# Kernel tuning notes

Hardware: AMD Instinct MI355X
Metric: run time of the kernel (lower is better)

Reference implementation:

```python
import jax, jax.numpy as jnp
import numpy as np

HEADS = 8
DIM_HEAD = 64

def setup_inputs() -> dict:
    key = jax.random.key(0)
    k1, k2, k3 = jax.random.split(key, 3)
    B, L, D = 8, 4096, 512
    hidden = HEADS * DIM_HEAD  # 512
    x = jax.random.normal(k1, (B, L, D), dtype=jnp.float32)
    # Conv1d(kernel_size=1) weights, squeezed to 2D matrices
    Wqkv = jax.random.normal(k2, (3 * hidden, D), dtype=jnp.float32) * (1.0 / np.sqrt(D))
    Wout = jax.random.normal(k3, (D, hidden), dtype=jnp.float32) * (1.0 / np.sqrt(hidden))
    bout = jnp.zeros((D,), dtype=jnp.float32)
    return {"x": x, "Wqkv": Wqkv, "Wout": Wout, "bout": bout}

def reference(x, Wqkv, Wout, bout):
    B, L, D = x.shape
    H, C = HEADS, DIM_HEAD
    # pointwise conv == linear over channel dim: (b, 3*H*C, l)
    qkv = jnp.einsum('bld,od->bol', x, Wqkv)
    qkv = qkv.reshape(B, 3, H, C, L)  # channel split order: (qkv, heads, c)
    q, k, v = qkv[:, 0], qkv[:, 1], qkv[:, 2]  # each (b, h, c, l)
    k = jax.nn.softmax(k, axis=-1)   # softmax over sequence
    q = jax.nn.softmax(q, axis=-2)   # softmax over feature dim (q_norm=True)
    context = jnp.einsum('bhdn,bhen->bhde', k, v)   # (b,h,c,c)
    out = jnp.einsum('bhde,bhdn->bhen', context, q)  # (b,h,c,l)
    out = out.reshape(B, H * C, L)
    y = jnp.einsum('bcl,dc->bld', out, Wout) + bout  # to_out + permute back
    return y
```

## Files before the change

kernel.cpp:

```cpp
#include <hip/hip_runtime.h>

#define L 4096
#define D 512
#define NCH 16

typedef __bf16 bf16x8 __attribute__((ext_vector_type(8)));
typedef float  f32x4  __attribute__((ext_vector_type(4)));

__device__ __forceinline__ void load_lds16(const void* g, void* l) {
    __builtin_amdgcn_global_load_lds(
        (const __attribute__((address_space(1))) void*)g,
        (__attribute__((address_space(3))) void*)l, 16, 0, 0);
}

__device__ __forceinline__ void barrier_mem() {
    asm volatile("" ::: "memory");
    __builtin_amdgcn_s_barrier();
    asm volatile("" ::: "memory");
}

#define NX8  (8 * 4096 * 512 / 8)
#define NW18 (1536 * 512 / 8)
#define NW28 (512 * 512 / 8)
__global__ __launch_bounds__(256) void convert_all(const float* __restrict__ x,
                                                   const float* __restrict__ Wq,
                                                   const float* __restrict__ Wo,
                                                   __bf16* __restrict__ dst) {
    int i = blockIdx.x * 256 + threadIdx.x;
    if (i >= NX8 + NW18 + NW28) return;
    const float* s;
    if (i < NX8)             s = x  + (size_t)i * 8;
    else if (i < NX8 + NW18) s = Wq + (size_t)(i - NX8) * 8;
    else                     s = Wo + (size_t)(i - NX8 - NW18) * 8;
    float4 a = ((const float4*)s)[0], b = ((const float4*)s)[1];
    bf16x8 o = {(__bf16)a.x, (__bf16)a.y, (__bf16)a.z, (__bf16)a.w,
                (__bf16)b.x, (__bf16)b.y, (__bf16)b.z, (__bf16)b.w};
    *(bf16x8*)(dst + (size_t)i * 8) = o;
}

template <int M, int N, int K, typename CT>
__global__ __launch_bounds__(512, 2) void gemm_bf16_256(
    const __bf16* __restrict__ A, size_t aStride,
    const __bf16* __restrict__ B, size_t bStride,
    CT* __restrict__ C, size_t cStride,
    const float* __restrict__ bias) {
    __shared__ __align__(16) __bf16 sA[2][256 * 64];
    __shared__ __align__(16) __bf16 sB[2][256 * 64];
    const int b  = blockIdx.z;
    const int m0 = blockIdx.y * 256;
    const int n0 = blockIdx.x * 256;
    const int t    = threadIdx.x;
    const int wave = t >> 6, lane = t & 63;
    const int wm = (wave >> 2) * 128;
    const int wn = (wave & 3) * 64;
    const int fr = lane & 15, g = lane >> 4;
    const __bf16* Ab = A + (size_t)b * aStride;
    const __bf16* Bb = B + (size_t)b * bStride;
    CT* Cb = C + (size_t)b * cStride;

    f32x4 acc[8][4];
#pragma unroll
    for (int i = 0; i < 8; i++)
#pragma unroll
        for (int j = 0; j < 4; j++) acc[i][j] = (f32x4)(0.0f);

    constexpr int NT = K / 64;

    auto stage2 = [&](int it, int kt, int pb) {
        const int idx = it * 512 + t;
        const int row = idx >> 3, cc = idx & 7;
        const int scc = cc ^ (row & 7);
        const size_t off = (size_t)row * K + (size_t)kt * 64 + scc * 8;
        load_lds16(Ab + (size_t)m0 * K + off, &sA[pb][idx * 8]);
        load_lds16(Bb + (size_t)n0 * K + off, &sB[pb][idx * 8]);
    };
    auto rdA4 = [&](bf16x8* dst, int pb, int ib, int kh) {
#pragma unroll
        for (int i = 0; i < 4; ++i) {
            const int row = wm + (ib + i) * 16 + fr;
            dst[i] = *(const bf16x8*)&sA[pb][row * 64 + (((kh << 2) + g) ^ (fr & 7)) * 8];
        }
    };
    auto rdB4 = [&](bf16x8* dst, int pb, int kh) {
#pragma unroll
        for (int j = 0; j < 4; ++j) {
            const int row = wn + j * 16 + fr;
            dst[j] = *(const bf16x8*)&sB[pb][row * 64 + (((kh << 2) + g) ^ (fr & 7)) * 8];
        }
    };
    auto mm16 = [&](const bf16x8* af, const bf16x8* bfr, int ib) {
        __builtin_amdgcn_s_setprio(1);
#pragma unroll
        for (int i = 0; i < 4; ++i)
#pragma unroll
            for (int j = 0; j < 4; ++j)
                acc[ib + i][j] = __builtin_amdgcn_mfma_f32_16x16x32_bf16(
                    af[i], bfr[j], acc[ib + i][j], 0, 0, 0);
        __builtin_amdgcn_s_setprio(0);
    };

#pragma unroll
    for (int it = 0; it < 4; ++it) stage2(it, 0, 0);

    for (int kt = 0; kt < NT; ++kt) {
        const int p = kt & 1;
        const bool pf = (kt + 1 < NT);
        bf16x8 bl[4], bh[4], al[4], ah[4], al2[4], ah2[4];

        if (pf) {
            stage2(0, kt + 1, p ^ 1);
            asm volatile("s_waitcnt vmcnt(2)" ::: "memory");
        } else {
            asm volatile("s_waitcnt vmcnt(0)" ::: "memory");
        }
        barrier_mem();
        rdB4(bl, p, 0);
        rdA4(al, p, 0, 0);
        rdA4(ah, p, 4, 0);
        asm volatile("s_waitcnt lgkmcnt(4)" ::: "memory");
        __builtin_amdgcn_sched_barrier(0);
        mm16(al, bl, 0);
        if (pf) stage2(1, kt + 1, p ^ 1);
        barrier_mem();

        rdB4(bh, p, 1);
        rdA4(al2, p, 0, 1);
        asm volatile("s_waitcnt lgkmcnt(8)" ::: "memory");
        __builtin_amdgcn_sched_barrier(0);
        mm16(ah, bl, 4);
        if (pf) stage2(2, kt + 1, p ^ 1);
        barrier_mem();

        rdA4(ah2, p, 4, 1);
        asm volatile("s_waitcnt lgkmcnt(4)" ::: "memory");
        __builtin_amdgcn_sched_barrier(0);
        mm16(al2, bh, 0);
        if (pf) stage2(3, kt + 1, p ^ 1);
        barrier_mem();

        asm volatile("s_waitcnt lgkmcnt(0)" ::: "memory");
        __builtin_amdgcn_sched_barrier(0);
        mm16(ah2, bh, 4);
        barrier_mem();
    }

    const int rb = g * 4;
#pragma unroll
    for (int j = 0; j < 4; ++j) {
        const int n = n0 + wn + j * 16 + fr;
        const float bv = bias ? bias[n] : 0.0f;
#pragma unroll
        for (int i = 0; i < 8; ++i) {
#pragma unroll
            for (int r = 0; r < 4; ++r) {
                const int m = m0 + wm + i * 16 + rb + r;
                Cb[(size_t)m * N + n] = (CT)(acc[i][j][r] + bv);
            }
        }
    }
}

__global__ __launch_bounds__(256) void kstats(const __bf16* __restrict__ qkv,
                                              float2* __restrict__ stats) {
    const int r = blockIdx.x;
    const int b = r >> 9, hc = r & 511;
    const __bf16* row = qkv + (size_t)b * 1536 * L + (size_t)(512 + hc) * L;
    __shared__ float sred[4];
    const int t = threadIdx.x;
    const bf16x8* p = (const bf16x8*)row;
    bf16x8 c0 = p[t * 2], c1 = p[t * 2 + 1];
    float v[16];
    float m = -1e30f;
#pragma unroll
    for (int j = 0; j < 8; j++) {
        v[j] = (float)c0[j];
        v[8 + j] = (float)c1[j];
    }
#pragma unroll
    for (int j = 0; j < 16; j++) m = fmaxf(m, v[j]);
#pragma unroll
    for (int off = 32; off > 0; off >>= 1) m = fmaxf(m, __shfl_down(m, off, 64));
    if ((t & 63) == 0) sred[t >> 6] = m;
    __syncthreads();
    const float m4 = fmaxf(fmaxf(sred[0], sred[1]), fmaxf(sred[2], sred[3]));
    float s = 0.f;
#pragma unroll
    for (int j = 0; j < 16; j++) s += __expf(v[j] - m4);
#pragma unroll
    for (int off = 32; off > 0; off >>= 1) s += __shfl_down(s, off, 64);
    __syncthreads();
    if ((t & 63) == 0) sred[t >> 6] = s;
    __syncthreads();
    if (t == 0) {
        const float stot = sred[0] + sred[1] + sred[2] + sred[3];
        stats[r] = make_float2(m4, 1.0f / stot);
    }
}

#define SKS 264
__global__ __launch_bounds__(256) void context_mfma(const __bf16* __restrict__ qkv,
                                                    const float2* __restrict__ stats,
                                                    float* __restrict__ ctxp) {
    __shared__ __align__(16) __bf16 smem[2 * 64 * SKS];
    __shared__ float smax[64];
    __bf16* sk = smem;
    __bf16* sv = smem + 64 * SKS;
    const int chunk = blockIdx.x;
    const int bh = blockIdx.y;
    const int b = bh >> 3, h = bh & 7;
    const __bf16* kbase = qkv + (size_t)b * 1536 * L + (size_t)(512 + h * 64) * L;
    const __bf16* vbase = qkv + (size_t)b * 1536 * L + (size_t)(1024 + h * 64) * L;
    const int t = threadIdx.x;
    if (t < 64) smax[t] = stats[bh * 64 + t].x;
    __syncthreads();

    {
        const int d = t >> 2, noff = (t & 3) * 64;
        const int n0 = chunk * 256;
        const __bf16* kp = kbase + (size_t)d * L + n0 + noff;
        const __bf16* vp = vbase + (size_t)d * L + n0 + noff;
        const float md = smax[d];
#pragma unroll
        for (int c = 0; c < 8; c++) {
            bf16x8 kk = *(const bf16x8*)(kp + c * 8);
            bf16x8 vv = *(const bf16x8*)(vp + c * 8);
            bf16x8 ek;
#pragma unroll
            for (int j = 0; j < 8; j++) ek[j] = (__bf16)__expf((float)kk[j] - md);
            *(bf16x8*)&sk[d * SKS + noff + c * 8] = ek;
            *(bf16x8*)&sv[d * SKS + noff + c * 8] = vv;
        }
    }
    __syncthreads();

    const int wave = t >> 6, lane = t & 63;
    const int fr = lane & 15, kq = (lane >> 4) * 8;
    f32x4 acc[4][4];
#pragma unroll
    for (int i = 0; i < 4; i++)
#pragma unroll
        for (int j = 0; j < 4; j++) acc[i][j] = (f32x4)(0.0f);
#pragma unroll
    for (int kh = 0; kh < 2; kh++) {
        const int koff = wave * 64 + kh * 32 + kq;
        bf16x8 af[4], bfr[4];
#pragma unroll
        for (int i = 0; i < 4; i++) {
            af[i]  = *(const bf16x8*)&sk[(i * 16 + fr) * SKS + koff];
            bfr[i] = *(const bf16x8*)&sv[(i * 16 + fr) * SKS + koff];
        }
#pragma unroll
        for (int i = 0; i < 4; i++)
#pragma unroll
            for (int j = 0; j < 4; j++)
                acc[i][j] = __builtin_amdgcn_mfma_f32_16x16x32_bf16(af[i], bfr[j], acc[i][j], 0, 0, 0);
    }
    __syncthreads();

    float* red = (float*)smem;
    const int col = lane & 15, rbase = (lane >> 4) * 4;
#pragma unroll
    for (int i = 0; i < 4; i++)
#pragma unroll
        for (int j = 0; j < 4; j++)
#pragma unroll
            for (int r = 0; r < 4; r++) {
                const int dd = i * 16 + rbase + r;
                const int ee = j * 16 + col;
                red[wave * 4096 + dd * 64 + ee] = acc[i][j][r];
            }
    __syncthreads();
    float* cp = ctxp + ((size_t)chunk * 64 + bh) * 4096;
#pragma unroll
    for (int gg = 0; gg < 4; gg++) {
        const int idx = t * 16 + gg * 4;
        f32x4 s = *(const f32x4*)&red[idx];
        s += *(const f32x4*)&red[4096 + idx];
        s += *(const f32x4*)&red[8192 + idx];
        s += *(const f32x4*)&red[12288 + idx];
        *(f32x4*)&cp[idx] = s;
    }
}

__global__ __launch_bounds__(256) void ctx_reduce(const float* __restrict__ ctxp,
                                                  const float2* __restrict__ stats,
                                                  __bf16* __restrict__ ctxT) {
    const int bh = blockIdx.x >> 2, quarter = blockIdx.x & 3;
    const int t = threadIdx.x;
    const int flat = quarter * 1024 + t * 4;
    const int d = flat >> 6, e0 = flat & 63;
    f32x4 s = (f32x4)(0.0f);
    for (int ch = 0; ch < NCH; ch++)
        s += *(const f32x4*)&ctxp[((size_t)ch * 64 + bh) * 4096 + flat];
    const float inv = stats[bh * 64 + d].y;
    __bf16* o = ctxT + (size_t)bh * 4096;
#pragma unroll
    for (int j = 0; j < 4; j++) o[(e0 + j) * 64 + d] = (__bf16)(s[j] * inv);
}

#define SPS 66
__global__ __launch_bounds__(256) void pv_fused(__bf16* __restrict__ qkv,
                                                const __bf16* __restrict__ ctxT) {
    __shared__ __align__(16) __bf16 sp[256 * SPS];
    __shared__ __align__(16) __bf16 sctx[64 * SPS];
    __shared__ float sinv[256];
    const int tileN = blockIdx.x;
    const int bh = blockIdx.y;
    const int b = bh >> 3, h = bh & 7;
    const int t = threadIdx.x;
    const int n0 = tileN * 256;
    const __bf16* qbase = qkv + (size_t)b * 1536 * L + (size_t)(h * 64) * L;

    {
        const int e = t >> 2, c = t & 3;
        const bf16x8* src = (const bf16x8*)(ctxT + ((size_t)bh * 64 + e) * 64 + c * 16);
        *(bf16x8*)&sctx[e * SPS + c * 16] = src[0];
        *(bf16x8*)&sctx[e * SPS + c * 16 + 8] = src[1];
    }

    float m = -1e30f;
    float qv[64];
#pragma unroll
    for (int d = 0; d < 64; d++) {
        qv[d] = (float)qbase[(size_t)d * L + n0 + t];
        m = fmaxf(m, qv[d]);
    }
    float s = 0.f;
#pragma unroll
    for (int d0 = 0; d0 < 64; d0 += 8) {
        bf16x8 ek;
#pragma unroll
        for (int j = 0; j < 8; j++) {
            float e = __expf(qv[d0 + j] - m);
            s += e;
            ek[j] = (__bf16)e;
        }
        *(bf16x8*)&sp[t * SPS + d0] = ek;
    }
    sinv[t] = 1.0f / s;
    __syncthreads();

    const int wave = t >> 6, lane = t & 63;
    const int wm = wave * 64;
    const int fr = lane & 15, kq = (lane >> 4) * 8;
    f32x4 acc[4][4];
#pragma unroll
    for (int i = 0; i < 4; i++)
#pragma unroll
        for (int j = 0; j < 4; j++) acc[i][j] = (f32x4)(0.0f);
#pragma unroll
    for (int kh = 0; kh < 2; kh++) {
        bf16x8 af[4], bfr[4];
#pragma unroll
        for (int i = 0; i < 4; i++)
            af[i] = *(const bf16x8*)&sp[(wm + i * 16 + fr) * SPS + kh * 32 + kq];
#pragma unroll
        for (int j = 0; j < 4; j++)
            bfr[j] = *(const bf16x8*)&sctx[(j * 16 + fr) * SPS + kh * 32 + kq];
#pragma unroll
        for (int i = 0; i < 4; i++)
#pragma unroll
            for (int j = 0; j < 4; j++)
                acc[i][j] = __builtin_amdgcn_mfma_f32_16x16x32_bf16(af[i], bfr[j], acc[i][j], 0, 0, 0);
    }

    __bf16* ob = qkv + (size_t)b * 1536 * L + (size_t)512 * L;
    const int col = lane & 15, rbase = (lane >> 4) * 4;
#pragma unroll
    for (int i = 0; i < 4; i++) {
#pragma unroll
        for (int r = 0; r < 4; r++) {
            const int nl = wm + i * 16 + rbase + r;
            const float inv = sinv[nl];
            const size_t rowoff = (size_t)(n0 + nl) * 512 + h * 64;
#pragma unroll
            for (int j = 0; j < 4; j++)
                ob[rowoff + j * 16 + col] = (__bf16)(acc[i][j][r] * inv);
        }
    }
}

extern "C" void kernel_launch(void* const* d_in, const int* in_sizes, int n_in,
                              void* d_out, int out_size, void* d_ws, size_t ws_size,
                              hipStream_t stream) {
    const float* x    = (const float*)d_in[0];
    const float* Wqkv = (const float*)d_in[1];
    const float* Wout = (const float*)d_in[2];
    const float* bout = (const float*)d_in[3];
    float* y = (float*)d_out;

    __bf16* qkv   = (__bf16*)d_ws;
    float*  ctxp  = (float*)(qkv + (size_t)8 * 1536 * L);
    __bf16* xb    = (__bf16*)(ctxp + (size_t)NCH * 64 * 4096);
    __bf16* Wqb   = xb + (size_t)8 * 4096 * 512;
    __bf16* Wob   = Wqb + (size_t)1536 * 512;
    float2* stats = (float2*)(Wob + (size_t)512 * 512);
    __bf16* ctxT  = (__bf16*)(stats + 4096);

    const int convBlocks = (NX8 + NW18 + NW28 + 255) / 256;
    convert_all<<<dim3(convBlocks), 256, 0, stream>>>(x, Wqkv, Wout, xb);

    gemm_bf16_256<1536, 4096, 512, __bf16><<<dim3(4096 / 256, 1536 / 256, 8), 512, 0, stream>>>(
        Wqb, 0, xb, (size_t)4096 * 512, qkv, (size_t)1536 * 4096, nullptr);

    kstats<<<dim3(4096), 256, 0, stream>>>(qkv, stats);
    context_mfma<<<dim3(NCH, 64), 256, 0, stream>>>(qkv, stats, ctxp);
    ctx_reduce<<<dim3(256), 256, 0, stream>>>(ctxp, stats, ctxT);
    pv_fused<<<dim3(L / 256, 64), 256, 0, stream>>>(qkv, ctxT);

    const __bf16* outT = qkv + (size_t)512 * L;
    gemm_bf16_256<4096, 512, 512, float><<<dim3(512 / 256, 4096 / 256, 8), 512, 0, stream>>>(
        outT, (size_t)1536 * L, Wob, 0, y, (size_t)4096 * 512, bout);
}
```

Before: 298.9 us.

## Restructure GEMM mainloop into 4-slot K=32 ring with 3-deep prefetch

```diff
diff --git a/kernel.cpp b/kernel.cpp
--- a/kernel.cpp
+++ b/kernel.cpp
@@ -44,8 +44,9 @@
     const __bf16* __restrict__ B, size_t bStride,
     CT* __restrict__ C, size_t cStride,
     const float* __restrict__ bias) {
-    __shared__ __align__(16) __bf16 sA[2][256 * 64];
-    __shared__ __align__(16) __bf16 sB[2][256 * 64];
+    __shared__ __align__(16) __bf16 sA[4][256 * 32];
+    __shared__ __align__(16) __bf16 sB[4][256 * 32];
+    constexpr int NQ = K / 32;
     const int b  = blockIdx.z;
     const int m0 = blockIdx.y * 256;
     const int n0 = blockIdx.x * 256;
@@ -54,8 +55,8 @@
     const int wm = (wave >> 2) * 128;
     const int wn = (wave & 3) * 64;
     const int fr = lane & 15, g = lane >> 4;
-    const __bf16* Ab = A + (size_t)b * aStride;
-    const __bf16* Bb = B + (size_t)b * bStride;
+    const __bf16* Ab = A + (size_t)b * aStride + (size_t)m0 * K;
+    const __bf16* Bb = B + (size_t)b * bStride + (size_t)n0 * K;
     CT* Cb = C + (size_t)b * cStride;
 
     f32x4 acc[8][4];
@@ -64,98 +65,74 @@
 #pragma unroll
         for (int j = 0; j < 4; j++) acc[i][j] = (f32x4)(0.0f);
 
-    constexpr int NT = K / 64;
-
-    auto stage2 = [&](int it, int kt, int pb) {
-        const int idx = it * 512 + t;
-        const int row = idx >> 3, cc = idx & 7;
-        const int scc = cc ^ (row & 7);
-        const size_t off = (size_t)row * K + (size_t)kt * 64 + scc * 8;
-        load_lds16(Ab + (size_t)m0 * K + off, &sA[pb][idx * 8]);
-        load_lds16(Bb + (size_t)n0 * K + off, &sB[pb][idx * 8]);
+    auto stageU = [&](const __bf16* Pb, int q, __bf16* slot) {
+#pragma unroll
+        for (int it = 0; it < 2; ++it) {
+            const int gi = it * 512 + t;
+            const int row = gi >> 2, cc = gi & 3;
+            const int scc = cc ^ ((row >> 1) & 3);
+            load_lds16(Pb + (size_t)row * K + q * 32 + scc * 8, slot + gi * 8);
+        }
     };
-    auto rdA4 = [&](bf16x8* dst, int pb, int ib, int kh) {
-#pragma unroll
-        for (int i = 0; i < 4; ++i) {
-            const int row = wm + (ib + i) * 16 + fr;
-            dst[i] = *(const bf16x8*)&sA[pb][row * 64 + (((kh << 2) + g) ^ (fr & 7)) * 8];
-        }
+    auto rdFrag = [&](const __bf16* slot, int rowbase) -> bf16x8 {
+        const int row = rowbase + fr;
+        return *(const bf16x8*)&slot[row * 32 + ((g ^ ((row >> 1) & 3)) * 8)];
     };
-    auto rdB4 = [&](bf16x8* dst, int pb, int kh) {
-#pragma unroll
-        for (int j = 0; j < 4; ++j) {
-            const int row = wn + j * 16 + fr;
-            dst[j] = *(const bf16x8*)&sB[pb][row * 64 + (((kh << 2) + g) ^ (fr & 7)) * 8];
-        }
-    };
-    auto mm16 = [&](const bf16x8* af, const bf16x8* bfr, int ib) {
-        __builtin_amdgcn_s_setprio(1);
-#pragma unroll
-        for (int i = 0; i < 4; ++i)
-#pragma unroll
-            for (int j = 0; j < 4; ++j)
-                acc[ib + i][j] = __builtin_amdgcn_mfma_f32_16x16x32_bf16(
-                    af[i], bfr[j], acc[ib + i][j], 0, 0, 0);
-        __builtin_amdgcn_s_setprio(0);
-    };
-
-#pragma unroll
-    for (int it = 0; it < 4; ++it) stage2(it, 0, 0);
-
-    for (int kt = 0; kt < NT; ++kt) {
-        const int p = kt & 1;
-        const bool pf = (kt + 1 < NT);
-        bf16x8 bl[4], bh[4], al[4], ah[4], al2[4], ah2[4];
-
-        if (pf) {
-            stage2(0, kt + 1, p ^ 1);
-            asm volatile("s_waitcnt vmcnt(2)" ::: "memory");
-        } else {
-            asm volatile("s_waitcnt vmcnt(0)" ::: "memory");
-        }
+
+    stageU(Bb, 0, sB[0]); stageU(Ab, 0, sA[0]);
+    stageU(Bb, 1, sB[1]); stageU(Ab, 1, sA[1]);
+    stageU(Bb, 2, sB[2]); stageU(Ab, 2, sA[2]);
+
+    for (int q = 0; q < NQ; ++q) {
+        const int sl = q & 3;
+        const __bf16* sAq = sA[sl];
+        const __bf16* sBq = sB[sl];
+        if (q <= NQ - 3)      asm volatile("s_waitcnt vmcnt(8)" ::: "memory");
+        else if (q == NQ - 2) asm volatile("s_waitcnt vmcnt(4)" ::: "memory");
+        else                  asm volatile("s_waitcnt vmcnt(0)" ::: "memory");
         barrier_mem();
-        rdB4(bl, p, 0);
-        rdA4(al, p, 0, 0);
-        rdA4(ah, p, 4, 0);
+        if (q + 3 < NQ) stageU(Bb, q + 3, sB[(q + 3) & 3]);
+        bf16x8 bfr[4], a0[4], a1[4];
+#pragma unroll
+        for (int j = 0; j < 4; ++j) bfr[j] = rdFrag(sBq, wn + j * 16);
+#pragma unroll
+        for (int i = 0; i < 4; ++i) a0[i] = rdFrag(sAq, wm + i * 16);
+#pragma unroll
+        for (int i = 0; i < 4; ++i) a1[i] = rdFrag(sAq, wm + 64 + i * 16);
+        if (q + 3 < NQ) stageU(Ab, q + 3, sA[(q + 3) & 3]);
         asm volatile("s_waitcnt lgkmcnt(4)" ::: "memory");
         __builtin_amdgcn_sched_barrier(0);
-        mm16(al, bl, 0);
-        if (pf) stage2(1, kt + 1, p ^ 1);
-        barrier_mem();
-
-        rdB4(bh, p, 1);
-        rdA4(al2, p, 0, 1);
-        asm volatile("s_waitcnt lgkmcnt(8)" ::: "memory");
-        __builtin_amdgcn_sched_barrier(0);
-        mm16(ah, bl, 4);
-        if (pf) stage2(2, kt + 1, p ^ 1);
-        barrier_mem();
-
-        rdA4(ah2, p, 4, 1);
-        asm volatile("s_waitcnt lgkmcnt(4)" ::: "memory");
-        __builtin_amdgcn_sched_barrier(0);
-        mm16(al2, bh, 0);
-        if (pf) stage2(3, kt + 1, p ^ 1);
-        barrier_mem();
-
+        __builtin_amdgcn_s_setprio(1);
+#pragma unroll
+        for (int i = 0; i < 4; ++i)
+#pragma unroll
+            for (int j = 0; j < 4; ++j)
+                acc[i][j] = __builtin_amdgcn_mfma_f32_16x16x32_bf16(a0[i], bfr[j], acc[i][j], 0, 0, 0);
+        __builtin_amdgcn_s_setprio(0);
         asm volatile("s_waitcnt lgkmcnt(0)" ::: "memory");
         __builtin_amdgcn_sched_barrier(0);
-        mm16(ah2, bh, 4);
-        barrier_mem();
+        __builtin_amdgcn_s_setprio(1);
+#pragma unroll
+        for (int i = 0; i < 4; ++i)
+#pragma unroll
+            for (int j = 0; j < 4; ++j)
+                acc[4 + i][j] = __builtin_amdgcn_mfma_f32_16x16x32_bf16(a1[i], bfr[j], acc[4 + i][j], 0, 0, 0);
+        __builtin_amdgcn_s_setprio(0);
     }
 
     const int rb = g * 4;
-#pragma unroll
-    for (int j = 0; j < 4; ++j) {
-        const int n = n0 + wn + j * 16 + fr;
-        const float bv = bias ? bias[n] : 0.0f;
-#pragma unroll
-        for (int i = 0; i < 8; ++i) {
-#pragma unroll
-            for (int r = 0; r < 4; ++r) {
-                const int m = m0 + wm + i * 16 + rb + r;
-                Cb[(size_t)m * N + n] = (CT)(acc[i][j][r] + bv);
-            }
+    float bv[4];
+#pragma unroll
+    for (int j = 0; j < 4; ++j) bv[j] = bias ? bias[n0 + wn + j * 16 + fr] : 0.0f;
+#pragma unroll
+    for (int i = 0; i < 8; ++i) {
+#pragma unroll
+        for (int r = 0; r < 4; ++r) {
+            const int m = m0 + wm + i * 16 + rb + r;
+            CT* rowp = Cb + (size_t)m * N + n0 + wn + fr;
+#pragma unroll
+            for (int j = 0; j < 4; ++j)
+                rowp[j * 16] = (CT)(acc[i][j][r] + bv[j]);
         }
     }
 }
```

After: 271.4 us. -9.2%, faster.
